# Performance work log

Measured on AMD Instinct MI355X. Metric: run time of the kernel, lower is better.

The kernel has to match this reference:

```python
import jax, jax.numpy as jnp
import numpy as np

B, S, D, H = 2, 4096, 256, 8
P = 64               # proj_dim_l
R = S // P           # proj_dim_r = 64, P*R == S
DH = D // H          # head_dim = 32


def setup_inputs() -> dict:
    key = jax.random.key(0)
    kx, kl, kr, kv, ko = jax.random.split(key, 5)
    scale = 0.05  # stand-in for xavier-uniform scale
    x  = jax.random.normal(kx, (B, S, D), dtype=jnp.float32)
    Wl = jax.random.normal(kl, (D, P), dtype=jnp.float32) * scale
    Wr = jax.random.normal(kr, (D, R), dtype=jnp.float32) * scale
    Wv = jax.random.normal(kv, (D, D), dtype=jnp.float32) * scale
    Wo = jax.random.normal(ko, (D, D), dtype=jnp.float32) * scale
    return {"x": x, "Wl": Wl, "Wr": Wr, "Wv": Wv, "Wo": Wo}


def reference(x, Wl, Wr, Wv, Wo):
    b, s, d = x.shape
    # value projection + head split -> (b, H, S, DH). Dropout p=0 (eval) = identity.
    v = (x @ Wv).reshape(b, s, H, DH).transpose(0, 2, 1, 3)
    # factorized score: row n is vec(outer(l_n, r_n)) of length P*R == S
    l = x @ Wl                                   # (b, S, P)
    r = x @ Wr                                   # (b, S, R)
    attn = (l[:, :, :, None] * r[:, :, None, :]).reshape(b, s, s)  # (b, S, S)
    score = jax.nn.softmax(attn, axis=-1)        # (b, S, S)
    # shared score across heads, per-head value matmul
    o = jnp.einsum('bnm,bhmd->bhnd', score, v)   # (b, H, S, DH)
    o = o.transpose(0, 2, 1, 3).reshape(b, s, d) # concat heads
    return o @ Wo
```

## Files before the change

### kernel.cpp

```cpp
#include <hip/hip_runtime.h>
#include <hip/hip_bf16.h>

typedef __attribute__((ext_vector_type(8))) __bf16 bf16x8;
typedef __attribute__((ext_vector_type(4))) __bf16 bf16x4;
typedef __attribute__((ext_vector_type(4))) float  f32x4;

#define MFMA16(a, b, c) __builtin_amdgcn_mfma_f32_16x16x32_bf16((a), (b), (c), 0, 0, 0)

static constexpr size_t OFF_WVT  = 0;
static constexpr size_t OFF_WLT  = OFF_WVT + 256 * 256 * 2;
static constexpr size_t OFF_WRT  = OFF_WLT + 64 * 256 * 2;
static constexpr size_t OFF_VT   = 1u << 20;
static constexpr size_t OFF_L    = 6u << 20;
static constexpr size_t OFF_R    = 8u << 20;
static constexpr size_t OFF_PART = 10u << 20;
static constexpr size_t OFF_ZP   = 26u << 20;

__device__ __forceinline__ float fast_exp2(float x) {
  float e;
  asm("v_exp_f32 %0, %1" : "=v"(e) : "v"(x));
  return e;
}

__device__ __forceinline__ bf16x8 cvt8(float4 a, float4 b) {
  bf16x8 o;
  o[0] = (__bf16)a.x; o[1] = (__bf16)a.y; o[2] = (__bf16)a.z; o[3] = (__bf16)a.w;
  o[4] = (__bf16)b.x; o[5] = (__bf16)b.y; o[6] = (__bf16)b.z; o[7] = (__bf16)b.w;
  return o;
}

__device__ __forceinline__ void gll16(const __bf16* g, __bf16* l) {
  __builtin_amdgcn_global_load_lds((const __attribute__((address_space(1))) void*)g,
                                   (__attribute__((address_space(3))) void*)l,
                                   16, 0, 0);
}

__global__ __launch_bounds__(1024) void k_prepw(const float* __restrict__ Wv,
                                                const float* __restrict__ Wl,
                                                const float* __restrict__ Wr,
                                                const float* __restrict__ Wo,
                                                __bf16* __restrict__ Wvt,
                                                __bf16* __restrict__ Wlt,
                                                __bf16* __restrict__ Wrt) {
  __shared__ float red[3][256];
  const int blk = blockIdx.x;
  const int t = threadIdx.x;
  if (blk < 32) {
    const int idx = blk * 1024 + t;
    if (idx < 16384) {
      const int k = idx >> 6, n = idx & 63;
      Wlt[n * 256 + k] = (__bf16)Wl[idx];
    } else {
      const int j = idx - 16384;
      const int k = j >> 6, n = j & 63;
      Wrt[n * 256 + k] = (__bf16)Wr[j];
    }
  } else {
    const int k  = blk - 32;
    const int n  = t & 255;
    const int jq = t >> 8;
    const float* wvr = Wv + (size_t)k * 256 + jq * 64;
    const float* wor = Wo + (size_t)(jq * 64) * 256 + n;
    float a0 = 0.f, a1 = 0.f, a2 = 0.f, a3 = 0.f;
#pragma unroll 4
    for (int j = 0; j < 64; j += 4) {
      a0 += wvr[j + 0] * wor[(size_t)(j + 0) * 256];
      a1 += wvr[j + 1] * wor[(size_t)(j + 1) * 256];
      a2 += wvr[j + 2] * wor[(size_t)(j + 2) * 256];
      a3 += wvr[j + 3] * wor[(size_t)(j + 3) * 256];
    }
    const float s = (a0 + a1) + (a2 + a3);
    if (jq > 0) red[jq - 1][n] = s;
    __syncthreads();
    if (jq == 0)
      Wvt[(size_t)n * 256 + k] = (__bf16)(s + red[0][n] + red[1][n] + red[2][n]);
  }
}

__global__ __launch_bounds__(256) void k_proj(const float* __restrict__ x,
                                              const __bf16* __restrict__ Wvt,
                                              const __bf16* __restrict__ Wlt,
                                              const __bf16* __restrict__ Wrt,
                                              __bf16* __restrict__ Vt,
                                              float* __restrict__ lbuf,
                                              float* __restrict__ rbuf) {
  __shared__ __align__(16) __bf16 vs[8 * 64 * 8];
  const int t = threadIdx.x;
  const int lane = t & 63, wave = t >> 6;
  const int l16 = lane & 15, quad = lane >> 4;
  const int wr = wave >> 1, wc = wave & 1;
  const int bid = blockIdx.x;
  const int q   = bid / 48;
  const int rmd = bid - q * 48;
  const int ct  = rmd >> 3;
  const int rbk = q * 8 + (rmd & 7);
  const __bf16* Wt;
  int colbase;
  if (ct < 4)       { Wt = Wvt; colbase = ct * 64; }
  else if (ct == 4) { Wt = Wlt; colbase = 0; }
  else              { Wt = Wrt; colbase = 0; }
  const int row0 = rbk * 64 + wr * 32;
  const int c0   = colbase + wc * 32;
  f32x4 acc[2][2] = {};
  for (int kk = 0; kk < 256; kk += 32) {
    const int ko = kk + quad * 8;
    const float* xr0 = x + (size_t)(row0 + l16) * 256 + ko;
    const float* xr1 = x + (size_t)(row0 + 16 + l16) * 256 + ko;
    bf16x8 a0 = cvt8(*(const float4*)xr0, *(const float4*)(xr0 + 4));
    bf16x8 a1 = cvt8(*(const float4*)xr1, *(const float4*)(xr1 + 4));
    bf16x8 b0 = *(const bf16x8*)(Wt + (size_t)(c0 + l16) * 256 + ko);
    bf16x8 b1 = *(const bf16x8*)(Wt + (size_t)(c0 + 16 + l16) * 256 + ko);
    acc[0][0] = MFMA16(a0, b0, acc[0][0]);
    acc[0][1] = MFMA16(a0, b1, acc[0][1]);
    acc[1][0] = MFMA16(a1, b0, acc[1][0]);
    acc[1][1] = MFMA16(a1, b1, acc[1][1]);
  }
  if (ct < 4) {
#pragma unroll
    for (int mt = 0; mt < 2; ++mt)
#pragma unroll
      for (int nt = 0; nt < 2; ++nt) {
        const int m8 = wr * 4 + mt * 2 + (quad >> 1);
        const int d  = wc * 32 + nt * 16 + l16;
        bf16x4 o;
        o.x = (__bf16)acc[mt][nt][0];
        o.y = (__bf16)acc[mt][nt][1];
        o.z = (__bf16)acc[mt][nt][2];
        o.w = (__bf16)acc[mt][nt][3];
        *(bf16x4*)(&vs[m8 * 512 + d * 8 + (quad & 1) * 4]) = o;
      }
    __syncthreads();
    const int m8 = t >> 5, s32 = t & 31;
    const int bat = rbk >> 6, mc = rbk & 63;
    bf16x8 a = *(const bf16x8*)(&vs[m8 * 512 + s32 * 16]);
    bf16x8 b = *(const bf16x8*)(&vs[m8 * 512 + s32 * 16 + 8]);
    __bf16* dst = Vt + (size_t)bat * 1048576 + (size_t)mc * 16384 +
                  m8 * 2048 + ct * 512 + s32 * 16;
    *(bf16x8*)dst       = a;
    *(bf16x8*)(dst + 8) = b;
  } else {
    float* dstb = (ct == 4) ? lbuf : rbuf;
#pragma unroll
    for (int mt = 0; mt < 2; ++mt)
#pragma unroll
      for (int nt = 0; nt < 2; ++nt) {
        const int col = c0 + nt * 16 + l16;
        const int gr  = rbk * 64 + wr * 32 + mt * 16 + quad * 4;
#pragma unroll
        for (int rr = 0; rr < 4; ++rr)
          dstb[(size_t)(gr + rr) * 64 + col] = acc[mt][nt][rr];
      }
  }
}

__global__ __launch_bounds__(256, 2) void k_attn(const float* __restrict__ lbuf,
                                                 const float* __restrict__ rbuf,
                                                 const __bf16* __restrict__ Vt,
                                                 __bf16* __restrict__ part,
                                                 float* __restrict__ zpart) {
  __shared__ __align__(16) char smem[69888];
  __bf16* vb0 = (__bf16*)smem;
  __bf16* vb1 = (__bf16*)(smem + 16384);
  __bf16* vb2 = (__bf16*)(smem + 32768);
  __bf16* vb3 = (__bf16*)(smem + 49152);
  float*  ls  = (float*)(smem + 65536);
  const int t = threadIdx.x;
  const int lane = t & 63, w = t >> 6;
  const int l16 = lane & 15, quad = lane >> 4;
  const int wr = w >> 1, wc = w & 1;
  const int bid = blockIdx.x;
  const int cmb = bid & 7;
  const int sp  = cmb >> 1;
  const int bat = cmb & 1;
  const int rbl = bid >> 3;
  const int g0  = bat * 4096 + rbl * 64;
  const __bf16* Vbase = Vt + (size_t)bat * 1048576;
  const int ck0 = sp * 32;

  {
    const int row = t >> 2, c = (t & 3) * 4;
    f32x4 v = *(const f32x4*)(lbuf + (size_t)(g0 + row) * 64 + sp * 16 + c);
    ls[row * 17 + c + 0] = v[0];
    ls[row * 17 + c + 1] = v[1];
    ls[row * 17 + c + 2] = v[2];
    ls[row * 17 + c + 3] = v[3];
  }
  const float LOG2E = 1.44269504088896f;
  float rreg[2][16];
#pragma unroll
  for (int mt = 0; mt < 2; ++mt) {
    const float* rp = rbuf + (size_t)(g0 + wr * 32 + mt * 16 + l16) * 64;
    f32x4 a = *(const f32x4*)(rp + quad * 8);
    f32x4 b = *(const f32x4*)(rp + quad * 8 + 4);
    f32x4 c = *(const f32x4*)(rp + 32 + quad * 8);
    f32x4 d = *(const f32x4*)(rp + 32 + quad * 8 + 4);
#pragma unroll
    for (int j = 0; j < 4; ++j) {
      rreg[mt][j]      = a[j] * LOG2E;
      rreg[mt][4 + j]  = b[j] * LOG2E;
      rreg[mt][8 + j]  = c[j] * LOG2E;
      rreg[mt][12 + j] = d[j] * LOG2E;
    }
  }

  f32x4 acc[2][8] = {};
  float zacc[2][2] = {{0.f, 0.f}, {0.f, 0.f}};

#define STAGE(KC, DST)                                                          \
  {                                                                             \
    const __bf16* src = Vbase + (size_t)(ck0 + (KC)) * 8192;                    \
    _Pragma("unroll")                                                           \
    for (int i = 0; i < 4; ++i)                                                 \
      gll16(src + (size_t)(i * 256 + t) * 8, (DST) + (i * 256 + (w << 6)) * 8); \
  }

#define AF_COMPUTE(KC)                                                        \
  {                                                                           \
    const int c16 = (KC) >> 1, hf = ((KC) & 1) * 8;                           \
    _Pragma("unroll")                                                         \
    for (int mt = 0; mt < 2; ++mt) {                                          \
      const float lv = ls[(wr * 32 + mt * 16 + l16) * 17 + c16];              \
      _Pragma("unroll")                                                       \
      for (int j = 0; j < 8; ++j) {                                           \
        const float e = fast_exp2(lv * rreg[mt][hf + j]);                     \
        zacc[mt][(KC) & 1] += e;                                              \
        af[mt][j] = (__bf16)e;                                                \
      }                                                                       \
    }                                                                         \
  }

#define MFMA_PHASE(CUR)                                                       \
  {                                                                           \
    _Pragma("unroll")                                                         \
    for (int nt = 0; nt < 8; ++nt) {                                          \
      bf16x8 bv = *(const bf16x8*)((CUR) + quad * 2048 +                      \
                                   (wc * 128 + nt * 16 + l16) * 8);           \
      acc[0][nt] = MFMA16(af[0], bv, acc[0][nt]);                             \
      acc[1][nt] = MFMA16(af[1], bv, acc[1][nt]);                             \
    }                                                                         \
  }

#define STEP(CC, BCUR, SC, BST, VM)                                           \
  {                                                                           \
    STAGE(SC, BST);                                                           \
    bf16x8 af[2];                                                             \
    AF_COMPUTE(CC);                                                           \
    asm volatile("s_waitcnt vmcnt(" #VM ")" ::: "memory");                    \
    __builtin_amdgcn_s_barrier();                                             \
    __builtin_amdgcn_sched_barrier(0);                                        \
    MFMA_PHASE(BCUR);                                                         \
    __builtin_amdgcn_s_barrier();                                             \
    __builtin_amdgcn_sched_barrier(0);                                        \
  }

#define STEPX(CC, BCUR, VM)                                                   \
  {                                                                           \
    bf16x8 af[2];                                                             \
    AF_COMPUTE(CC);                                                           \
    asm volatile("s_waitcnt vmcnt(" #VM ")" ::: "memory");                    \
    __builtin_amdgcn_s_barrier();                                             \
    __builtin_amdgcn_sched_barrier(0);                                        \
    MFMA_PHASE(BCUR);                                                         \
    __builtin_amdgcn_s_barrier();                                             \
    __builtin_amdgcn_sched_barrier(0);                                        \
  }

  STAGE(0, vb0);
  STAGE(1, vb1);
  STAGE(2, vb2);
  __syncthreads();

  for (int c = 0; c < 28; c += 4) {
    STEP(c + 0, vb0, c + 3, vb3, 12);
    STEP(c + 1, vb1, c + 4, vb0, 12);
    STEP(c + 2, vb2, c + 5, vb1, 12);
    STEP(c + 3, vb3, c + 6, vb2, 12);
  }
  STEP (28, vb0, 31, vb3, 12);
  STEPX(29, vb1, 8);
  STEPX(30, vb2, 4);
  STEPX(31, vb3, 0);

#undef STAGE
#undef AF_COMPUTE
#undef MFMA_PHASE
#undef STEP
#undef STEPX

#pragma unroll
  for (int mt = 0; mt < 2; ++mt) {
    float z = zacc[mt][0] + zacc[mt][1];
    z += __shfl_xor(z, 16);
    z += __shfl_xor(z, 32);
    if (wc == 0 && quad == 0)
      zpart[(size_t)sp * 8192 + g0 + wr * 32 + mt * 16 + l16] = z;
  }

  __syncthreads();
  __bf16* ctile = (__bf16*)smem;
#pragma unroll
  for (int mt = 0; mt < 2; ++mt)
#pragma unroll
    for (int nt = 0; nt < 8; ++nt) {
      const int r0 = wr * 32 + mt * 16 + quad * 4;
      const int c  = wc * 128 + nt * 16 + l16;
#pragma unroll
      for (int rr = 0; rr < 4; ++rr)
        ctile[(r0 + rr) * 264 + c] = (__bf16)acc[mt][nt][rr];
    }
  __syncthreads();
  __bf16* pb = part + (size_t)sp * (8192 * 256);
#pragma unroll
  for (int p = 0; p < 8; ++p) {
    const int u = p * 256 + t;
    const int row = u >> 5, seg = u & 31;
    *(bf16x8*)(pb + (size_t)(g0 + row) * 256 + seg * 8) =
        *(const bf16x8*)(ctile + row * 264 + seg * 8);
  }
}

__global__ __launch_bounds__(256) void k_fix(const __bf16* __restrict__ part,
                                             const float* __restrict__ zpart,
                                             float* __restrict__ out) {
  const int idx = blockIdx.x * 256 + threadIdx.x;
  const int g = idx >> 5, seg = idx & 31;
  float z = 0.f;
#pragma unroll
  for (int s = 0; s < 4; ++s) z += zpart[(size_t)s * 8192 + g];
  const float iz = 1.0f / z;
  float sum[8] = {};
#pragma unroll
  for (int s = 0; s < 4; ++s) {
    bf16x8 p = *(const bf16x8*)(part + (size_t)s * (8192 * 256) + (size_t)g * 256 + seg * 8);
#pragma unroll
    for (int j = 0; j < 8; ++j) sum[j] += (float)p[j];
  }
  f32x4 o0, o1;
#pragma unroll
  for (int j = 0; j < 4; ++j) { o0[j] = sum[j] * iz; o1[j] = sum[4 + j] * iz; }
  float* dst = out + (size_t)g * 256 + seg * 8;
  *(f32x4*)dst       = o0;
  *(f32x4*)(dst + 4) = o1;
}

extern "C" void kernel_launch(void* const* d_in, const int* in_sizes, int n_in,
                              void* d_out, int out_size, void* d_ws, size_t ws_size,
                              hipStream_t stream) {
  const float* x  = (const float*)d_in[0];
  const float* Wl = (const float*)d_in[1];
  const float* Wr = (const float*)d_in[2];
  const float* Wv = (const float*)d_in[3];
  const float* Wo = (const float*)d_in[4];
  char* ws = (char*)d_ws;
  __bf16* Wvt = (__bf16*)(ws + OFF_WVT);
  __bf16* Wlt = (__bf16*)(ws + OFF_WLT);
  __bf16* Wrt = (__bf16*)(ws + OFF_WRT);
  __bf16* Vt  = (__bf16*)(ws + OFF_VT);
  float*  lb  = (float*)(ws + OFF_L);
  float*  rbf = (float*)(ws + OFF_R);
  __bf16* prt = (__bf16*)(ws + OFF_PART);
  float*  zp  = (float*)(ws + OFF_ZP);
  float*  out = (float*)d_out;

  k_prepw<<<288, 1024, 0, stream>>>(Wv, Wl, Wr, Wo, Wvt, Wlt, Wrt);
  k_proj<<<768, 256, 0, stream>>>(x, Wvt, Wlt, Wrt, Vt, lb, rbf);
  k_attn<<<512, 256, 0, stream>>>(lb, rbf, Vt, prt, zp);
  k_fix<<<1024, 256, 0, stream>>>(prt, zp, out);
}
```

Before: 121.0 us.

## Fuse all four kernels into one persistent kernel with grid barriers

Replaces the four separate launches (weight prep, projection, attention, normalization fix) with a single 512-block persistent kernel that separates the stages with atomic-counter grid barriers, plus a memset of the barrier counters. The goal is to remove launch gaps and tail effects between kernels. To fit shared memory for two blocks per CU, the attention V pipeline drops from four stages to three, which reduces prefetch depth. The Wv·Wo precompute now runs one 256-thread block per row, giving it less parallelism. The grid barrier depends on all 512 blocks being co-resident, which the launch bounds are meant to guarantee.

```diff
diff --git a/kernel.cpp b/kernel.cpp
--- a/kernel.cpp
+++ b/kernel.cpp
@@ -15,6 +15,7 @@
 static constexpr size_t OFF_R    = 8u << 20;
 static constexpr size_t OFF_PART = 10u << 20;
 static constexpr size_t OFF_ZP   = 26u << 20;
+static constexpr size_t OFF_BAR  = 27u << 20;
 
 __device__ __forceinline__ float fast_exp2(float x) {
   float e;
@@ -35,63 +36,58 @@
                                    16, 0, 0);
 }
 
-__global__ __launch_bounds__(1024) void k_prepw(const float* __restrict__ Wv,
-                                                const float* __restrict__ Wl,
-                                                const float* __restrict__ Wr,
-                                                const float* __restrict__ Wo,
-                                                __bf16* __restrict__ Wvt,
-                                                __bf16* __restrict__ Wlt,
-                                                __bf16* __restrict__ Wrt) {
-  __shared__ float red[3][256];
-  const int blk = blockIdx.x;
-  const int t = threadIdx.x;
-  if (blk < 32) {
-    const int idx = blk * 1024 + t;
+__device__ __forceinline__ void gbar(unsigned* c, unsigned tgt) {
+  __syncthreads();
+  if (threadIdx.x == 0) {
+    __threadfence();
+    atomicAdd(c, 1u);
+    while (__hip_atomic_load(c, __ATOMIC_RELAXED, __HIP_MEMORY_SCOPE_AGENT) < tgt)
+      __builtin_amdgcn_s_sleep(2);
+    __threadfence();
+  }
+  __syncthreads();
+}
+
+__device__ __forceinline__ void dev_wvo(int k, int t, const float* __restrict__ Wv,
+                                        const float* __restrict__ Wo,
+                                        __bf16* __restrict__ Wvt) {
+  const float* wvr = Wv + (size_t)k * 256;
+  const float* wo  = Wo + t;
+  float a[8] = {};
+  for (int j = 0; j < 256; j += 8) {
+#pragma unroll
+    for (int u = 0; u < 8; ++u) a[u] += wvr[j + u] * wo[(size_t)(j + u) * 256];
+  }
+  const float s = ((a[0] + a[1]) + (a[2] + a[3])) + ((a[4] + a[5]) + (a[6] + a[7]));
+  Wvt[(size_t)t * 256 + k] = (__bf16)s;
+}
+
+__device__ __forceinline__ void dev_tr(int base, int t, const float* __restrict__ Wl,
+                                       const float* __restrict__ Wr,
+                                       __bf16* __restrict__ Wlt, __bf16* __restrict__ Wrt) {
+#pragma unroll
+  for (int i = 0; i < 4; ++i) {
+    const int idx = base + i * 256 + t;
     if (idx < 16384) {
-      const int k = idx >> 6, n = idx & 63;
-      Wlt[n * 256 + k] = (__bf16)Wl[idx];
+      Wlt[(idx & 63) * 256 + (idx >> 6)] = (__bf16)Wl[idx];
     } else {
       const int j = idx - 16384;
-      const int k = j >> 6, n = j & 63;
-      Wrt[n * 256 + k] = (__bf16)Wr[j];
+      Wrt[(j & 63) * 256 + (j >> 6)] = (__bf16)Wr[j];
     }
-  } else {
-    const int k  = blk - 32;
-    const int n  = t & 255;
-    const int jq = t >> 8;
-    const float* wvr = Wv + (size_t)k * 256 + jq * 64;
-    const float* wor = Wo + (size_t)(jq * 64) * 256 + n;
-    float a0 = 0.f, a1 = 0.f, a2 = 0.f, a3 = 0.f;
-#pragma unroll 4
-    for (int j = 0; j < 64; j += 4) {
-      a0 += wvr[j + 0] * wor[(size_t)(j + 0) * 256];
-      a1 += wvr[j + 1] * wor[(size_t)(j + 1) * 256];
-      a2 += wvr[j + 2] * wor[(size_t)(j + 2) * 256];
-      a3 += wvr[j + 3] * wor[(size_t)(j + 3) * 256];
-    }
-    const float s = (a0 + a1) + (a2 + a3);
-    if (jq > 0) red[jq - 1][n] = s;
-    __syncthreads();
-    if (jq == 0)
-      Wvt[(size_t)n * 256 + k] = (__bf16)(s + red[0][n] + red[1][n] + red[2][n]);
-  }
-}
-
-__global__ __launch_bounds__(256) void k_proj(const float* __restrict__ x,
-                                              const __bf16* __restrict__ Wvt,
-                                              const __bf16* __restrict__ Wlt,
-                                              const __bf16* __restrict__ Wrt,
-                                              __bf16* __restrict__ Vt,
-                                              float* __restrict__ lbuf,
-                                              float* __restrict__ rbuf) {
-  __shared__ __align__(16) __bf16 vs[8 * 64 * 8];
-  const int t = threadIdx.x;
+  }
+}
+
+__device__ void dev_proj(int u, int t, char* smem_, const float* __restrict__ x,
+                         const __bf16* __restrict__ Wvt, const __bf16* __restrict__ Wlt,
+                         const __bf16* __restrict__ Wrt, __bf16* __restrict__ Vt,
+                         float* __restrict__ lbuf, float* __restrict__ rbuf) {
+  __bf16* vs = (__bf16*)smem_;
+  __syncthreads();
   const int lane = t & 63, wave = t >> 6;
   const int l16 = lane & 15, quad = lane >> 4;
   const int wr = wave >> 1, wc = wave & 1;
-  const int bid = blockIdx.x;
-  const int q   = bid / 48;
-  const int rmd = bid - q * 48;
+  const int q   = u / 48;
+  const int rmd = u - q * 48;
   const int ct  = rmd >> 3;
   const int rbk = q * 8 + (rmd & 7);
   const __bf16* Wt;
@@ -153,22 +149,16 @@
   }
 }
 
-__global__ __launch_bounds__(256, 2) void k_attn(const float* __restrict__ lbuf,
-                                                 const float* __restrict__ rbuf,
-                                                 const __bf16* __restrict__ Vt,
-                                                 __bf16* __restrict__ part,
-                                                 float* __restrict__ zpart) {
-  __shared__ __align__(16) char smem[69888];
-  __bf16* vb0 = (__bf16*)smem;
-  __bf16* vb1 = (__bf16*)(smem + 16384);
-  __bf16* vb2 = (__bf16*)(smem + 32768);
-  __bf16* vb3 = (__bf16*)(smem + 49152);
-  float*  ls  = (float*)(smem + 65536);
-  const int t = threadIdx.x;
+__device__ void dev_attn(int bid, int t, char* smem_, const float* __restrict__ lbuf,
+                         const float* __restrict__ rbuf, const __bf16* __restrict__ Vt,
+                         __bf16* __restrict__ part, float* __restrict__ zpart) {
+  __bf16* vb0 = (__bf16*)smem_;
+  __bf16* vb1 = (__bf16*)(smem_ + 16384);
+  __bf16* vb2 = (__bf16*)(smem_ + 32768);
+  float*  ls  = (float*)(smem_ + 49152);
   const int lane = t & 63, w = t >> 6;
   const int l16 = lane & 15, quad = lane >> 4;
   const int wr = w >> 1, wc = w & 1;
-  const int bid = blockIdx.x;
   const int cmb = bid & 7;
   const int sp  = cmb >> 1;
   const int bat = cmb & 1;
@@ -267,19 +257,15 @@
 
   STAGE(0, vb0);
   STAGE(1, vb1);
-  STAGE(2, vb2);
-  __syncthreads();
-
-  for (int c = 0; c < 28; c += 4) {
-    STEP(c + 0, vb0, c + 3, vb3, 12);
-    STEP(c + 1, vb1, c + 4, vb0, 12);
-    STEP(c + 2, vb2, c + 5, vb1, 12);
-    STEP(c + 3, vb3, c + 6, vb2, 12);
-  }
-  STEP (28, vb0, 31, vb3, 12);
-  STEPX(29, vb1, 8);
-  STEPX(30, vb2, 4);
-  STEPX(31, vb3, 0);
+  __syncthreads();
+
+  for (int c = 0; c < 30; c += 3) {
+    STEP(c + 0, vb0, c + 2, vb2, 8);
+    STEP(c + 1, vb1, c + 3, vb0, 8);
+    STEP(c + 2, vb2, c + 4, vb1, 8);
+  }
+  STEPX(30, vb0, 4);
+  STEPX(31, vb1, 0);
 
 #undef STAGE
 #undef AF_COMPUTE
@@ -297,7 +283,7 @@
   }
 
   __syncthreads();
-  __bf16* ctile = (__bf16*)smem;
+  __bf16* ctile = (__bf16*)smem_;
 #pragma unroll
   for (int mt = 0; mt < 2; ++mt)
 #pragma unroll
@@ -319,10 +305,9 @@
   }
 }
 
-__global__ __launch_bounds__(256) void k_fix(const __bf16* __restrict__ part,
-                                             const float* __restrict__ zpart,
-                                             float* __restrict__ out) {
-  const int idx = blockIdx.x * 256 + threadIdx.x;
+__device__ __forceinline__ void dev_fix(int idx, const __bf16* __restrict__ part,
+                                        const float* __restrict__ zpart,
+                                        float* __restrict__ out) {
   const int g = idx >> 5, seg = idx & 31;
   float z = 0.f;
 #pragma unroll
@@ -341,6 +326,34 @@
   float* dst = out + (size_t)g * 256 + seg * 8;
   *(f32x4*)dst       = o0;
   *(f32x4*)(dst + 4) = o1;
+}
+
+__global__ __launch_bounds__(256, 2) void k_mega(const float* __restrict__ x,
+                                                 const float* __restrict__ Wl,
+                                                 const float* __restrict__ Wr,
+                                                 const float* __restrict__ Wv,
+                                                 const float* __restrict__ Wo,
+                                                 __bf16* Wvt, __bf16* Wlt, __bf16* Wrt,
+                                                 __bf16* Vt, float* lbuf, float* rbuf,
+                                                 __bf16* part, float* zpart, float* out,
+                                                 unsigned* bar) {
+  __shared__ __align__(16) char smem[53504];
+  const int bid = blockIdx.x;
+  const int t   = threadIdx.x;
+
+  if (bid < 256)      dev_wvo(bid, t, Wv, Wo, Wvt);
+  else if (bid < 288) dev_tr((bid - 256) * 1024, t, Wl, Wr, Wlt, Wrt);
+  gbar(bar + 0, 512);
+
+  dev_proj(bid, t, smem, x, Wvt, Wlt, Wrt, Vt, lbuf, rbuf);
+  if (bid < 256) dev_proj(512 + bid, t, smem, x, Wvt, Wlt, Wrt, Vt, lbuf, rbuf);
+  gbar(bar + 16, 512);
+
+  dev_attn(bid, t, smem, lbuf, rbuf, Vt, part, zpart);
+  gbar(bar + 32, 512);
+
+  dev_fix(bid * 256 + t, part, zpart, out);
+  dev_fix((512 + bid) * 256 + t, part, zpart, out);
 }
 
 extern "C" void kernel_launch(void* const* d_in, const int* in_sizes, int n_in,
@@ -360,10 +373,10 @@
   float*  rbf = (float*)(ws + OFF_R);
   __bf16* prt = (__bf16*)(ws + OFF_PART);
   float*  zp  = (float*)(ws + OFF_ZP);
+  unsigned* bar = (unsigned*)(ws + OFF_BAR);
   float*  out = (float*)d_out;
 
-  k_prepw<<<288, 1024, 0, stream>>>(Wv, Wl, Wr, Wo, Wvt, Wlt, Wrt);
-  k_proj<<<768, 256, 0, stream>>>(x, Wvt, Wlt, Wrt, Vt, lb, rbf);
-  k_attn<<<512, 256, 0, stream>>>(lb, rbf, Vt, prt, zp);
-  k_fix<<<1024, 256, 0, stream>>>(prt, zp, out);
-}
+  hipMemsetAsync(bar, 0, 256, stream);
+  k_mega<<<512, 256, 0, stream>>>(x, Wl, Wr, Wv, Wo, Wvt, Wlt, Wrt, Vt,
+                                  lb, rbf, prt, zp, out, bar);
+}
```

Result: slower. 289.6 us (+139.3%).

## Fuse split-K reduction into attention kernel via last-block atomic counter

Applied to the files above, without the earlier changes.

Removes the separate k_fix launch. Each attention block increments a per-row-group atomic counter, and the last of the four split blocks sums the bf16 partials, normalises by the summed softmax denominators, and writes the output. It also stages the l/r projection results through shared memory so they go out as coalesced float4 stores. This trades a kernel launch and its scheduling gap for a memset, atomics, fences, and a serialized tail of reduction work in the last-arriving blocks.

```diff
diff --git a/kernel.cpp b/kernel.cpp
--- a/kernel.cpp
+++ b/kernel.cpp
@@ -15,6 +15,7 @@
 static constexpr size_t OFF_R    = 8u << 20;
 static constexpr size_t OFF_PART = 10u << 20;
 static constexpr size_t OFF_ZP   = 26u << 20;
+static constexpr size_t OFF_CNT  = 27u << 20;
 
 __device__ __forceinline__ float fast_exp2(float x) {
   float e;
@@ -84,7 +85,7 @@
                                               __bf16* __restrict__ Vt,
                                               float* __restrict__ lbuf,
                                               float* __restrict__ rbuf) {
-  __shared__ __align__(16) __bf16 vs[8 * 64 * 8];
+  __shared__ __align__(16) char smem[16896];
   const int t = threadIdx.x;
   const int lane = t & 63, wave = t >> 6;
   const int l16 = lane & 15, quad = lane >> 4;
@@ -116,6 +117,7 @@
     acc[1][1] = MFMA16(a1, b1, acc[1][1]);
   }
   if (ct < 4) {
+    __bf16* vs = (__bf16*)smem;
 #pragma unroll
     for (int mt = 0; mt < 2; ++mt)
 #pragma unroll
@@ -139,17 +141,29 @@
     *(bf16x8*)dst       = a;
     *(bf16x8*)(dst + 8) = b;
   } else {
+    float* lsf = (float*)smem;
+#pragma unroll
+    for (int mt = 0; mt < 2; ++mt)
+#pragma unroll
+      for (int nt = 0; nt < 2; ++nt) {
+        const int col = wc * 32 + nt * 16 + l16;
+        const int r0  = wr * 32 + mt * 16 + quad * 4;
+#pragma unroll
+        for (int rr = 0; rr < 4; ++rr)
+          lsf[(r0 + rr) * 65 + col] = acc[mt][nt][rr];
+      }
+    __syncthreads();
     float* dstb = (ct == 4) ? lbuf : rbuf;
-#pragma unroll
-    for (int mt = 0; mt < 2; ++mt)
-#pragma unroll
-      for (int nt = 0; nt < 2; ++nt) {
-        const int col = c0 + nt * 16 + l16;
-        const int gr  = rbk * 64 + wr * 32 + mt * 16 + quad * 4;
-#pragma unroll
-        for (int rr = 0; rr < 4; ++rr)
-          dstb[(size_t)(gr + rr) * 64 + col] = acc[mt][nt][rr];
-      }
+    const int row = t >> 2, cs = (t & 3) * 16;
+    const float* src = lsf + row * 65 + cs;
+    float* d = dstb + (size_t)(rbk * 64 + row) * 64 + cs;
+#pragma unroll
+    for (int v = 0; v < 4; ++v) {
+      f32x4 o;
+      o[0] = src[v * 4 + 0]; o[1] = src[v * 4 + 1];
+      o[2] = src[v * 4 + 2]; o[3] = src[v * 4 + 3];
+      *(f32x4*)(d + v * 4) = o;
+    }
   }
 }
 
@@ -157,7 +171,9 @@
                                                  const float* __restrict__ rbuf,
                                                  const __bf16* __restrict__ Vt,
                                                  __bf16* __restrict__ part,
-                                                 float* __restrict__ zpart) {
+                                                 float* __restrict__ zpart,
+                                                 unsigned* __restrict__ cnt,
+                                                 float* __restrict__ out) {
   __shared__ __align__(16) char smem[69888];
   __bf16* vb0 = (__bf16*)smem;
   __bf16* vb1 = (__bf16*)(smem + 16384);
@@ -174,6 +190,7 @@
   const int bat = cmb & 1;
   const int rbl = bid >> 3;
   const int g0  = bat * 4096 + rbl * 64;
+  const int rg  = bat * 64 + rbl;
   const __bf16* Vbase = Vt + (size_t)bat * 1048576;
   const int ck0 = sp * 32;
 
@@ -317,30 +334,41 @@
     *(bf16x8*)(pb + (size_t)(g0 + row) * 256 + seg * 8) =
         *(const bf16x8*)(ctile + row * 264 + seg * 8);
   }
-}
-
-__global__ __launch_bounds__(256) void k_fix(const __bf16* __restrict__ part,
-                                             const float* __restrict__ zpart,
-                                             float* __restrict__ out) {
-  const int idx = blockIdx.x * 256 + threadIdx.x;
-  const int g = idx >> 5, seg = idx & 31;
-  float z = 0.f;
-#pragma unroll
-  for (int s = 0; s < 4; ++s) z += zpart[(size_t)s * 8192 + g];
-  const float iz = 1.0f / z;
-  float sum[8] = {};
-#pragma unroll
-  for (int s = 0; s < 4; ++s) {
-    bf16x8 p = *(const bf16x8*)(part + (size_t)s * (8192 * 256) + (size_t)g * 256 + seg * 8);
-#pragma unroll
-    for (int j = 0; j < 8; ++j) sum[j] += (float)p[j];
-  }
-  f32x4 o0, o1;
-#pragma unroll
-  for (int j = 0; j < 4; ++j) { o0[j] = sum[j] * iz; o1[j] = sum[4 + j] * iz; }
-  float* dst = out + (size_t)g * 256 + seg * 8;
-  *(f32x4*)dst       = o0;
-  *(f32x4*)(dst + 4) = o1;
+
+  int* flag = (int*)(smem + 69632);
+  __syncthreads();
+  if (t == 0) {
+    __threadfence();
+    flag[0] = (int)atomicAdd(cnt + rg, 1u);
+  }
+  __syncthreads();
+  if (flag[0] == 3) {
+    __threadfence();
+#pragma unroll
+    for (int p = 0; p < 8; ++p) {
+      const int u = p * 256 + t;
+      const int row = g0 + (u >> 5);
+      const int seg = u & 31;
+      float z = 0.f;
+#pragma unroll
+      for (int s = 0; s < 4; ++s) z += zpart[(size_t)s * 8192 + row];
+      const float iz = 1.0f / z;
+      float sum[8] = {};
+#pragma unroll
+      for (int s = 0; s < 4; ++s) {
+        bf16x8 pv = *(const bf16x8*)(part + (size_t)s * (8192 * 256) +
+                                     (size_t)row * 256 + seg * 8);
+#pragma unroll
+        for (int j = 0; j < 8; ++j) sum[j] += (float)pv[j];
+      }
+      f32x4 o0, o1;
+#pragma unroll
+      for (int j = 0; j < 4; ++j) { o0[j] = sum[j] * iz; o1[j] = sum[4 + j] * iz; }
+      float* dst = out + (size_t)row * 256 + seg * 8;
+      *(f32x4*)dst       = o0;
+      *(f32x4*)(dst + 4) = o1;
+    }
+  }
 }
 
 extern "C" void kernel_launch(void* const* d_in, const int* in_sizes, int n_in,
@@ -360,10 +388,11 @@
   float*  rbf = (float*)(ws + OFF_R);
   __bf16* prt = (__bf16*)(ws + OFF_PART);
   float*  zp  = (float*)(ws + OFF_ZP);
+  unsigned* cnt = (unsigned*)(ws + OFF_CNT);
   float*  out = (float*)d_out;
 
+  hipMemsetAsync(cnt, 0, 512, stream);
   k_prepw<<<288, 1024, 0, stream>>>(Wv, Wl, Wr, Wo, Wvt, Wlt, Wrt);
   k_proj<<<768, 256, 0, stream>>>(x, Wvt, Wlt, Wrt, Vt, lb, rbf);
-  k_attn<<<512, 256, 0, stream>>>(lb, rbf, Vt, prt, zp);
-  k_fix<<<1024, 256, 0, stream>>>(prt, zp, out);
-}
+  k_attn<<<512, 256, 0, stream>>>(lb, rbf, Vt, prt, zp, cnt, out);
+}
```

Measured after the change: 184.8 us. +52.7%, slower.
